# Optimization experiments

Measured on AMD Instinct MI355X. Metric: run time of the kernel, lower is better.

Reference implementation:

```python
import jax, jax.numpy as jnp
import numpy as np

DIRECTIONS = [(0, 0), (1, 0), (-1, 0), (0, 1), (0, -1)]  # (dx, dy)
BN_EPS = 1e-5


def shift2d(x, directions=DIRECTIONS):
    # x: (B, C, H, W). Split channels into G groups, roll each spatially,
    # zero out the wrapped-around border (zero_pad mode), then concat.
    C = x.shape[1]
    G = len(directions)
    base = C // G
    sizes = [base] * (G - 1) + [C - base * (G - 1)]
    starts = np.concatenate([[0], np.cumsum(sizes)])
    out = []
    for i, (dx, dy) in enumerate(directions):
        chunk = x[:, starts[i]:starts[i + 1]]
        if dx == 0 and dy == 0:
            out.append(chunk)
            continue
        y = jnp.roll(chunk, shift=(dy, dx), axis=(-2, -1))
        if dy > 0:
            y = y.at[..., :dy, :].set(0.0)
        elif dy < 0:
            y = y.at[..., dy:, :].set(0.0)
        if dx > 0:
            y = y.at[..., :, :dx].set(0.0)
        elif dx < 0:
            y = y.at[..., :, dx:].set(0.0)
        out.append(y)
    return jnp.concatenate(out, axis=1)


def setup_inputs() -> dict:
    key = jax.random.key(0)
    k1, k2, k3, k4 = jax.random.split(key, 4)
    B, Cin, Cout, H, W = 32, 256, 256, 56, 56
    x = jax.random.normal(k1, (B, Cin, H, W), dtype=jnp.float32)
    pw_w = jax.random.normal(k2, (Cout, Cin), dtype=jnp.float32) * (1.0 / np.sqrt(Cin))
    gamma = jnp.ones((Cout,), dtype=jnp.float32)
    beta = jnp.zeros((Cout,), dtype=jnp.float32)
    running_mean = jax.random.normal(k3, (Cout,), dtype=jnp.float32) * 0.1
    running_var = jax.random.uniform(k4, (Cout,), dtype=jnp.float32, minval=0.5, maxval=1.5)
    return {"x": x, "pw_w": pw_w, "gamma": gamma, "beta": beta,
            "running_mean": running_mean, "running_var": running_var}


def reference(x, pw_w, gamma, beta, running_mean, running_var):
    # Shift (parameter-free spatial mixing)
    y = shift2d(x)
    # stride=1 -> down is Identity
    # 1x1 conv (no bias): pointwise channel mixing
    y = jnp.einsum('bchw,oc->bohw', y, pw_w)
    # BatchNorm2d (inference form with running stats) + ReLU
    inv = gamma * jax.lax.rsqrt(running_var + BN_EPS)
    y = y * inv[None, :, None, None] + (beta - running_mean * inv)[None, :, None, None]
    return jax.nn.relu(y)
```

## Files before the change

### kernel.cpp

```cpp
#include <hip/hip_runtime.h>

#define H_ 56
#define W_ 56
#define HW_ 3136
#define CIN_ 256
#define COUT_ 256

typedef __attribute__((ext_vector_type(8))) short short8;
typedef __attribute__((ext_vector_type(4))) float f32x4;

__device__ unsigned short g_wbf[COUT_ * CIN_];

__device__ __forceinline__ int swz32(int n) { return ((n ^ (n >> 3)) & 3) << 3; }

__device__ __forceinline__ unsigned short f2bf(float f) {
  union { float f; unsigned int i; } v; v.f = f;
  unsigned int b = v.i + (0x7fffu + ((v.i >> 16) & 1u));
  return (unsigned short)(b >> 16);
}

__device__ __forceinline__ void gload_lds16(const unsigned short* g, unsigned short* l) {
  __builtin_amdgcn_global_load_lds(
      (const __attribute__((address_space(1))) unsigned int*)g,
      (__attribute__((address_space(3))) unsigned int*)l, 16, 0, 0);
}

__device__ __forceinline__ void shift_decode(int c, int& dx, int& dy) {
  if (c < 102)      { dy = 0; dx = (c < 51) ? 0 : 1; }
  else if (c < 153) { dx = -1; dy = 0; }
  else if (c < 204) { dx = 0;  dy = 1; }
  else              { dx = 0;  dy = -1; }
}

__global__ __launch_bounds__(256)
void prep_weights(const float* __restrict__ wgt) {
  int idx  = blockIdx.x * 256 + threadIdx.x;
  int tile = idx >> 12;
  int bm = tile >> 3, kt = tile & 7;
  int e   = idx & 4095;
  int m   = e >> 5, col = e & 31;
  int o   = bm * 128 + m;
  int k   = kt * 32 + (col ^ swz32(m));
  g_wbf[idx] = f2bf(wgt[o * CIN_ + k]);
}

__device__ __forceinline__ void load_x(const float* __restrict__ x, size_t xb,
                                       int hh, int w0, int c,
                                       float4& p0, float4& p1, float& pe) {
  int dx, dy; shift_decode(c, dx, dy);
  int h2 = hh - dy;
  p0 = make_float4(0.f, 0.f, 0.f, 0.f);
  p1 = make_float4(0.f, 0.f, 0.f, 0.f);
  pe = 0.f;
  if ((unsigned)h2 < (unsigned)H_) {
    const float* row = x + xb + (size_t)c * HW_ + h2 * W_;
    p0 = *(const float4*)(row + w0);
    p1 = *(const float4*)(row + w0 + 4);
    if (dx == 1)       { if (w0 > 0)      pe = row[w0 - 1]; }
    else if (dx == -1) { if (w0 + 8 < W_) pe = row[w0 + 8]; }
  }
}

__device__ __forceinline__ void write_b(unsigned short* __restrict__ B,
                                        int nloc0, int krow, int c,
                                        const float4& p0, const float4& p1, float pe) {
  int dx, dy; shift_decode(c, dx, dy);
  float s[8] = {p0.x, p0.y, p0.z, p0.w, p1.x, p1.y, p1.z, p1.w};
  float vals[8];
  if (dx == 0) {
    #pragma unroll
    for (int i = 0; i < 8; ++i) vals[i] = s[i];
  } else if (dx == 1) {
    #pragma unroll
    for (int i = 7; i >= 1; --i) vals[i] = s[i - 1];
    vals[0] = pe;
  } else {
    #pragma unroll
    for (int i = 0; i < 7; ++i) vals[i] = s[i + 1];
    vals[7] = pe;
  }
  #pragma unroll
  for (int i = 0; i < 8; ++i) {
    int nl = nloc0 + i;
    B[nl * 32 + (krow ^ swz32(nl))] = f2bf(vals[i]);
  }
}

__global__ __launch_bounds__(256, 4)
void shiftconv_gemm(const float* __restrict__ x,
                    const float* __restrict__ gamma,
                    const float* __restrict__ beta,
                    const float* __restrict__ rmean,
                    const float* __restrict__ rvar,
                    float* __restrict__ out)
{
  __shared__ unsigned short Alds[2][128 * 32];
  __shared__ unsigned short Blds[2][64 * 32];
  __shared__ float bnp[256];

  const int t = threadIdx.x;
  const int orig = blockIdx.x;
  const int wgid = (orig & 7) * 392 + (orig >> 3);
  const int bm   = wgid & 1;
  const int bn   = wgid >> 1;

  const int lane = t & 63;
  const int wv   = t >> 6;
  const int wm   = wv >> 1;
  const int wn   = wv & 1;
  const int quad = lane >> 4;
  const int l15  = lane & 15;

  if (t < 128) {
    int o = bm * 128 + t;
    float inv = gamma[o] * rsqrtf(rvar[o] + 1e-5f);
    bnp[2 * t]     = inv;
    bnp[2 * t + 1] = beta[o] - rmean[o] * inv;
  }

  const int chunk  = t & 7;
  const int krow   = t >> 3;
  const int nloc0  = chunk * 8;
  const int nglob0 = bn * 64 + nloc0;
  const int bidx   = nglob0 / HW_;
  const int rem    = nglob0 - bidx * HW_;
  const int hh     = rem / W_;
  const int w0     = rem - hh * W_;
  const size_t xb  = (size_t)bidx * CIN_ * HW_;

  const unsigned short* wsrc = g_wbf + bm * (8 * 4096) + t * 8;

  f32x4 acc[4][2];
  #pragma unroll
  for (int i = 0; i < 4; ++i)
    #pragma unroll
    for (int j = 0; j < 2; ++j)
      acc[i][j] = (f32x4){0.f, 0.f, 0.f, 0.f};

  float4 p0, p1;
  float  pe;

  {
    const unsigned short* g = wsrc;
    gload_lds16(g,        &Alds[0][wv * 512]);
    gload_lds16(g + 2048, &Alds[0][wv * 512 + 2048]);
  }
  load_x(x, xb, hh, w0, krow, p0, p1, pe);
  write_b(&Blds[0][0], nloc0, krow, krow, p0, p1, pe);
  __syncthreads();

  const int kb = quad * 8;
  int buf = 0;

  for (int kt = 0; kt < 8; ++kt) {
    if (kt < 7) {
      const unsigned short* g = wsrc + (kt + 1) * 4096;
      gload_lds16(g,        &Alds[buf ^ 1][wv * 512]);
      gload_lds16(g + 2048, &Alds[buf ^ 1][wv * 512 + 2048]);
      load_x(x, xb, hh, w0, (kt + 1) * 32 + krow, p0, p1, pe);
    }

    short8 af[4], bfr[2];
    #pragma unroll
    for (int f = 0; f < 4; ++f) {
      int ml = wm * 64 + f * 16 + l15;
      af[f] = *(const short8*)(&Alds[buf][ml * 32 + (kb ^ swz32(ml))]);
    }
    #pragma unroll
    for (int g2 = 0; g2 < 2; ++g2) {
      int nl2 = wn * 32 + g2 * 16 + l15;
      bfr[g2] = *(const short8*)(&Blds[buf][nl2 * 32 + (kb ^ swz32(nl2))]);
    }
    #pragma unroll
    for (int mf = 0; mf < 4; ++mf)
      #pragma unroll
      for (int nf = 0; nf < 2; ++nf)
        acc[mf][nf] = __builtin_amdgcn_mfma_f32_16x16x32_bf16(
            af[mf], bfr[nf], acc[mf][nf], 0, 0, 0);

    if (kt < 7)
      write_b(&Blds[buf ^ 1][0], nloc0, krow, (kt + 1) * 32 + krow, p0, p1, pe);

    __syncthreads();
    buf ^= 1;
  }

  size_t nbase[2];
  #pragma unroll
  for (int nf = 0; nf < 2; ++nf) {
    int ng  = bn * 64 + wn * 32 + nf * 16 + l15;
    int b2  = ng / HW_;
    int hw2 = ng - b2 * HW_;
    nbase[nf] = (size_t)b2 * COUT_ * HW_ + hw2;
  }
  #pragma unroll
  for (int mf = 0; mf < 4; ++mf) {
    int mloc = wm * 64 + mf * 16 + quad * 4;
    float inv[4], add[4];
    #pragma unroll
    for (int r = 0; r < 4; ++r) {
      inv[r] = bnp[2 * (mloc + r)];
      add[r] = bnp[2 * (mloc + r) + 1];
    }
    size_t obase = (size_t)(bm * 128 + mloc) * HW_;
    #pragma unroll
    for (int nf = 0; nf < 2; ++nf) {
      #pragma unroll
      for (int r = 0; r < 4; ++r) {
        float v = fmaf(acc[mf][nf][r], inv[r], add[r]);
        out[nbase[nf] + obase + (size_t)r * HW_] = fmaxf(v, 0.0f);
      }
    }
  }
}

extern "C" void kernel_launch(void* const* d_in, const int* in_sizes, int n_in,
                              void* d_out, int out_size, void* d_ws, size_t ws_size,
                              hipStream_t stream) {
  const float* x     = (const float*)d_in[0];
  const float* wgt   = (const float*)d_in[1];
  const float* gamma = (const float*)d_in[2];
  const float* beta  = (const float*)d_in[3];
  const float* rmean = (const float*)d_in[4];
  const float* rvar  = (const float*)d_in[5];
  float* out = (float*)d_out;

  prep_weights<<<dim3(256), dim3(256), 0, stream>>>(wgt);
  shiftconv_gemm<<<dim3(3136), dim3(256), 0, stream>>>(x, gamma, beta, rmean, rvar, out);
}
```

Baseline: 210.3 us.

## Triple-buffer weight tiles and prefetch activations two K-steps ahead

Weight tiles in LDS go from double to triple buffering, and the K loop is unrolled by two so that activation registers for two future K-slices are in flight at once. __syncthreads is replaced by an explicit lgkmcnt wait plus s_barrier, with sched_barrier hints to keep the asynchronous global-to-LDS copies ahead of the register loads. The aim is to hide global memory latency in this latency-bound shifted-conv GEMM. The cost is more LDS per block, which could reduce occupancy. The barriers also lean on in-order vmcnt completion to make sure the LDS copies have landed before they are read.

```diff
diff --git a/kernel.cpp b/kernel.cpp
--- a/kernel.cpp
+++ b/kernel.cpp
@@ -94,7 +94,7 @@
                     const float* __restrict__ rvar,
                     float* __restrict__ out)
 {
-  __shared__ unsigned short Alds[2][128 * 32];
+  __shared__ unsigned short Alds[3][128 * 32];
   __shared__ unsigned short Blds[2][64 * 32];
   __shared__ float bnp[256];
 
@@ -137,52 +137,90 @@
     for (int j = 0; j < 2; ++j)
       acc[i][j] = (f32x4){0.f, 0.f, 0.f, 0.f};
 
-  float4 p0, p1;
-  float  pe;
-
-  {
-    const unsigned short* g = wsrc;
-    gload_lds16(g,        &Alds[0][wv * 512]);
-    gload_lds16(g + 2048, &Alds[0][wv * 512 + 2048]);
-  }
-  load_x(x, xb, hh, w0, krow, p0, p1, pe);
-  write_b(&Blds[0][0], nloc0, krow, krow, p0, p1, pe);
+  float4 pa0, pa1; float pea;
+  float4 pb0, pb1; float peb;
+
+  const int kb = quad * 8;
+
+  gload_lds16(wsrc,        &Alds[0][wv * 512]);
+  gload_lds16(wsrc + 2048, &Alds[0][wv * 512 + 2048]);
+  gload_lds16(wsrc + 4096, &Alds[1][wv * 512]);
+  gload_lds16(wsrc + 6144, &Alds[1][wv * 512 + 2048]);
+  __builtin_amdgcn_sched_barrier(0);
+  load_x(x, xb, hh, w0, krow, pa0, pa1, pea);
+  write_b(&Blds[0][0], nloc0, krow, krow, pa0, pa1, pea);
+  load_x(x, xb, hh, w0, 32 + krow, pb0, pb1, peb);
   __syncthreads();
 
-  const int kb = quad * 8;
-  int buf = 0;
-
-  for (int kt = 0; kt < 8; ++kt) {
-    if (kt < 7) {
-      const unsigned short* g = wsrc + (kt + 1) * 4096;
-      gload_lds16(g,        &Alds[buf ^ 1][wv * 512]);
-      gload_lds16(g + 2048, &Alds[buf ^ 1][wv * 512 + 2048]);
-      load_x(x, xb, hh, w0, (kt + 1) * 32 + krow, p0, p1, pe);
-    }
-
-    short8 af[4], bfr[2];
-    #pragma unroll
-    for (int f = 0; f < 4; ++f) {
-      int ml = wm * 64 + f * 16 + l15;
-      af[f] = *(const short8*)(&Alds[buf][ml * 32 + (kb ^ swz32(ml))]);
-    }
-    #pragma unroll
-    for (int g2 = 0; g2 < 2; ++g2) {
-      int nl2 = wn * 32 + g2 * 16 + l15;
-      bfr[g2] = *(const short8*)(&Blds[buf][nl2 * 32 + (kb ^ swz32(nl2))]);
-    }
-    #pragma unroll
-    for (int mf = 0; mf < 4; ++mf)
-      #pragma unroll
-      for (int nf = 0; nf < 2; ++nf)
-        acc[mf][nf] = __builtin_amdgcn_mfma_f32_16x16x32_bf16(
-            af[mf], bfr[nf], acc[mf][nf], 0, 0, 0);
-
-    if (kt < 7)
-      write_b(&Blds[buf ^ 1][0], nloc0, krow, (kt + 1) * 32 + krow, p0, p1, pe);
-
-    __syncthreads();
-    buf ^= 1;
+  for (int kt2 = 0; kt2 < 4; ++kt2) {
+    const int te     = 2 * kt2;
+    const int aCur   = te % 3;
+    const int aNext  = (te + 1) % 3;
+    const int aStage = (te + 2) % 3;
+
+    if (kt2 < 3) {
+      const unsigned short* g = wsrc + (te + 2) * 4096;
+      gload_lds16(g,        &Alds[aStage][wv * 512]);
+      gload_lds16(g + 2048, &Alds[aStage][wv * 512 + 2048]);
+      __builtin_amdgcn_sched_barrier(0);
+      load_x(x, xb, hh, w0, (te + 2) * 32 + krow, pa0, pa1, pea);
+    }
+    {
+      short8 af[4], bfr[2];
+      #pragma unroll
+      for (int f = 0; f < 4; ++f) {
+        int ml = wm * 64 + f * 16 + l15;
+        af[f] = *(const short8*)(&Alds[aCur][ml * 32 + (kb ^ swz32(ml))]);
+      }
+      #pragma unroll
+      for (int g2 = 0; g2 < 2; ++g2) {
+        int nl2 = wn * 32 + g2 * 16 + l15;
+        bfr[g2] = *(const short8*)(&Blds[0][nl2 * 32 + (kb ^ swz32(nl2))]);
+      }
+      #pragma unroll
+      for (int mf = 0; mf < 4; ++mf)
+        #pragma unroll
+        for (int nf = 0; nf < 2; ++nf)
+          acc[mf][nf] = __builtin_amdgcn_mfma_f32_16x16x32_bf16(
+              af[mf], bfr[nf], acc[mf][nf], 0, 0, 0);
+    }
+    write_b(&Blds[1][0], nloc0, krow, (te + 1) * 32 + krow, pb0, pb1, peb);
+    asm volatile("s_waitcnt lgkmcnt(0)" ::: "memory");
+    __builtin_amdgcn_s_barrier();
+    __builtin_amdgcn_sched_barrier(0);
+
+    if (kt2 < 3) {
+      const unsigned short* g = wsrc + (te + 3) * 4096;
+      gload_lds16(g,        &Alds[aCur][wv * 512]);
+      gload_lds16(g + 2048, &Alds[aCur][wv * 512 + 2048]);
+      __builtin_amdgcn_sched_barrier(0);
+      load_x(x, xb, hh, w0, (te + 3) * 32 + krow, pb0, pb1, peb);
+    }
+    {
+      short8 af[4], bfr[2];
+      #pragma unroll
+      for (int f = 0; f < 4; ++f) {
+        int ml = wm * 64 + f * 16 + l15;
+        af[f] = *(const short8*)(&Alds[aNext][ml * 32 + (kb ^ swz32(ml))]);
+      }
+      #pragma unroll
+      for (int g2 = 0; g2 < 2; ++g2) {
+        int nl2 = wn * 32 + g2 * 16 + l15;
+        bfr[g2] = *(const short8*)(&Blds[1][nl2 * 32 + (kb ^ swz32(nl2))]);
+      }
+      #pragma unroll
+      for (int mf = 0; mf < 4; ++mf)
+        #pragma unroll
+        for (int nf = 0; nf < 2; ++nf)
+          acc[mf][nf] = __builtin_amdgcn_mfma_f32_16x16x32_bf16(
+              af[mf], bfr[nf], acc[mf][nf], 0, 0, 0);
+    }
+    if (kt2 < 3) {
+      write_b(&Blds[0][0], nloc0, krow, (te + 2) * 32 + krow, pa0, pa1, pea);
+      asm volatile("s_waitcnt lgkmcnt(0)" ::: "memory");
+      __builtin_amdgcn_s_barrier();
+      __builtin_amdgcn_sched_barrier(0);
+    }
   }
 
   size_t nbase[2];
```

New measurement: 211.9 us. Within noise of the previous version (+0.8%).

## Widen GEMM block tile to all 256 output channels to avoid duplicate x loads

Applied to the files above, without the earlier changes.

Each workgroup now computes all 256 output channels for a 64-pixel tile instead of 128. Previously two workgroups loaded and converted the same shifted x slice. The weight prep layout is changed to match, and each wave now owns 64 rows by 64 columns with a 4x4 MFMA accumulator set. This halves global reads and bf16 conversion of the input, but doubles LDS for A and accumulator registers, lowers the occupancy hint to 3, and halves the grid to 1568 blocks.

```diff
diff --git a/kernel.cpp b/kernel.cpp
--- a/kernel.cpp
+++ b/kernel.cpp
@@ -34,14 +34,12 @@
 
 __global__ __launch_bounds__(256)
 void prep_weights(const float* __restrict__ wgt) {
-  int idx  = blockIdx.x * 256 + threadIdx.x;
-  int tile = idx >> 12;
-  int bm = tile >> 3, kt = tile & 7;
-  int e   = idx & 4095;
+  int idx = blockIdx.x * 256 + threadIdx.x;
+  int kt  = idx >> 13;
+  int e   = idx & 8191;
   int m   = e >> 5, col = e & 31;
-  int o   = bm * 128 + m;
   int k   = kt * 32 + (col ^ swz32(m));
-  g_wbf[idx] = f2bf(wgt[o * CIN_ + k]);
+  g_wbf[idx] = f2bf(wgt[m * CIN_ + k]);
 }
 
 __device__ __forceinline__ void load_x(const float* __restrict__ x, size_t xb,
@@ -86,7 +84,7 @@
   }
 }
 
-__global__ __launch_bounds__(256, 4)
+__global__ __launch_bounds__(256, 3)
 void shiftconv_gemm(const float* __restrict__ x,
                     const float* __restrict__ gamma,
                     const float* __restrict__ beta,
@@ -94,25 +92,22 @@
                     const float* __restrict__ rvar,
                     float* __restrict__ out)
 {
-  __shared__ unsigned short Alds[2][128 * 32];
+  __shared__ unsigned short Alds[2][256 * 32];
   __shared__ unsigned short Blds[2][64 * 32];
-  __shared__ float bnp[256];
+  __shared__ float bnp[512];
 
   const int t = threadIdx.x;
   const int orig = blockIdx.x;
-  const int wgid = (orig & 7) * 392 + (orig >> 3);
-  const int bm   = wgid & 1;
-  const int bn   = wgid >> 1;
+  const int bn   = (orig & 7) * 196 + (orig >> 3);
 
   const int lane = t & 63;
   const int wv   = t >> 6;
-  const int wm   = wv >> 1;
-  const int wn   = wv & 1;
+  const int wm   = wv;
   const int quad = lane >> 4;
   const int l15  = lane & 15;
 
-  if (t < 128) {
-    int o = bm * 128 + t;
+  {
+    int o = t;
     float inv = gamma[o] * rsqrtf(rvar[o] + 1e-5f);
     bnp[2 * t]     = inv;
     bnp[2 * t + 1] = beta[o] - rmean[o] * inv;
@@ -128,13 +123,13 @@
   const int w0     = rem - hh * W_;
   const size_t xb  = (size_t)bidx * CIN_ * HW_;
 
-  const unsigned short* wsrc = g_wbf + bm * (8 * 4096) + t * 8;
-
-  f32x4 acc[4][2];
+  const unsigned short* wsrc = g_wbf + t * 8;
+
+  f32x4 acc[4][4];
   #pragma unroll
   for (int i = 0; i < 4; ++i)
     #pragma unroll
-    for (int j = 0; j < 2; ++j)
+    for (int j = 0; j < 4; ++j)
       acc[i][j] = (f32x4){0.f, 0.f, 0.f, 0.f};
 
   float4 p0, p1;
@@ -142,8 +137,10 @@
 
   {
     const unsigned short* g = wsrc;
-    gload_lds16(g,        &Alds[0][wv * 512]);
-    gload_lds16(g + 2048, &Alds[0][wv * 512 + 2048]);
+    unsigned short* l = &Alds[0][t * 8];
+    #pragma unroll
+    for (int p = 0; p < 4; ++p)
+      gload_lds16(g + p * 2048, l + p * 2048);
   }
   load_x(x, xb, hh, w0, krow, p0, p1, pe);
   write_b(&Blds[0][0], nloc0, krow, krow, p0, p1, pe);
@@ -154,27 +151,29 @@
 
   for (int kt = 0; kt < 8; ++kt) {
     if (kt < 7) {
-      const unsigned short* g = wsrc + (kt + 1) * 4096;
-      gload_lds16(g,        &Alds[buf ^ 1][wv * 512]);
-      gload_lds16(g + 2048, &Alds[buf ^ 1][wv * 512 + 2048]);
+      const unsigned short* g = wsrc + (kt + 1) * 8192;
+      unsigned short* l = &Alds[buf ^ 1][t * 8];
+      #pragma unroll
+      for (int p = 0; p < 4; ++p)
+        gload_lds16(g + p * 2048, l + p * 2048);
       load_x(x, xb, hh, w0, (kt + 1) * 32 + krow, p0, p1, pe);
     }
 
-    short8 af[4], bfr[2];
+    short8 af[4], bfr[4];
     #pragma unroll
     for (int f = 0; f < 4; ++f) {
       int ml = wm * 64 + f * 16 + l15;
       af[f] = *(const short8*)(&Alds[buf][ml * 32 + (kb ^ swz32(ml))]);
     }
     #pragma unroll
-    for (int g2 = 0; g2 < 2; ++g2) {
-      int nl2 = wn * 32 + g2 * 16 + l15;
+    for (int g2 = 0; g2 < 4; ++g2) {
+      int nl2 = g2 * 16 + l15;
       bfr[g2] = *(const short8*)(&Blds[buf][nl2 * 32 + (kb ^ swz32(nl2))]);
     }
     #pragma unroll
     for (int mf = 0; mf < 4; ++mf)
       #pragma unroll
-      for (int nf = 0; nf < 2; ++nf)
+      for (int nf = 0; nf < 4; ++nf)
         acc[mf][nf] = __builtin_amdgcn_mfma_f32_16x16x32_bf16(
             af[mf], bfr[nf], acc[mf][nf], 0, 0, 0);
 
@@ -185,10 +184,10 @@
     buf ^= 1;
   }
 
-  size_t nbase[2];
-  #pragma unroll
-  for (int nf = 0; nf < 2; ++nf) {
-    int ng  = bn * 64 + wn * 32 + nf * 16 + l15;
+  size_t nbase[4];
+  #pragma unroll
+  for (int nf = 0; nf < 4; ++nf) {
+    int ng  = bn * 64 + nf * 16 + l15;
     int b2  = ng / HW_;
     int hw2 = ng - b2 * HW_;
     nbase[nf] = (size_t)b2 * COUT_ * HW_ + hw2;
@@ -202,9 +201,9 @@
       inv[r] = bnp[2 * (mloc + r)];
       add[r] = bnp[2 * (mloc + r) + 1];
     }
-    size_t obase = (size_t)(bm * 128 + mloc) * HW_;
-    #pragma unroll
-    for (int nf = 0; nf < 2; ++nf) {
+    size_t obase = (size_t)mloc * HW_;
+    #pragma unroll
+    for (int nf = 0; nf < 4; ++nf) {
       #pragma unroll
       for (int r = 0; r < 4; ++r) {
         float v = fmaf(acc[mf][nf][r], inv[r], add[r]);
@@ -226,5 +225,5 @@
   float* out = (float*)d_out;
 
   prep_weights<<<dim3(256), dim3(256), 0, stream>>>(wgt);
-  shiftconv_gemm<<<dim3(3136), dim3(256), 0, stream>>>(x, gamma, beta, rmean, rvar, out);
-}
+  shiftconv_gemm<<<dim3(1568), dim3(256), 0, stream>>>(x, gamma, beta, rmean, rvar, out);
+}
```

New measurement: 203.3 us. 1.03x faster.
